# Performance work log

Measured on AMD Instinct MI355X. Metric: run time of the kernel, lower is better.

The kernel has to match this reference:

```python
import jax, jax.numpy as jnp
import numpy as np

N = 50000   # nodes
E = 500000  # edges
H = 128     # hidden_dim


def setup_inputs() -> dict:
    key = jax.random.key(0)
    ks = jax.random.split(key, 8)
    w = lambda k, shp: jax.random.normal(k, shp, jnp.float32) * 0.02
    return {
        "edge_idx": jax.random.randint(ks[0], (E, 2), 0, N, dtype=jnp.int32),
        "node_feats": jax.random.normal(ks[1], (N, H), jnp.float32),
        "edge_feats": jax.random.normal(ks[2], (E, H), jnp.float32),
        # edge MLP params: Linear(3H,H) -> ReLU -> Linear(H,H) -> LayerNorm(H)
        "We1": w(ks[3], (3 * H, H)), "be1": jnp.zeros((H,), jnp.float32),
        "We2": w(ks[4], (H, H)),     "be2": jnp.zeros((H,), jnp.float32),
        "ge": jnp.ones((H,), jnp.float32), "bge": jnp.zeros((H,), jnp.float32),
        # node MLP params: Linear(2H,H) -> ReLU -> Linear(H,H) -> LayerNorm(H)
        "Wn1": w(ks[5], (2 * H, H)), "bn1": jnp.zeros((H,), jnp.float32),
        "Wn2": w(ks[6], (H, H)),     "bn2": jnp.zeros((H,), jnp.float32),
        "gn": jnp.ones((H,), jnp.float32), "bgn": jnp.zeros((H,), jnp.float32),
    }


def layer_norm(x, g, b, eps=1e-5):
    m = jnp.mean(x, axis=-1, keepdims=True)
    v = jnp.var(x, axis=-1, keepdims=True)
    return (x - m) * jax.lax.rsqrt(v + eps) * g + b


def reference(edge_idx, node_feats, edge_feats,
              We1, be1, We2, be2, ge, bge,
              Wn1, bn1, Wn2, bn2, gn, bgn):
    senders = edge_idx[:, 0]
    receivers = edge_idx[:, 1]
    # edge update: gather endpoints, concat with edge feats, MLP + LN
    e_in = jnp.concatenate([node_feats[senders], node_feats[receivers], edge_feats], axis=-1)  # [E, 3H]
    edge_update = layer_norm(jax.nn.relu(e_in @ We1 + be1) @ We2 + be2, ge, bge)               # [E, H]
    # faithful to source: scatter-add of edge_feats (NOT edge_update) into receivers
    acc = jax.ops.segment_sum(edge_feats, receivers, num_segments=node_feats.shape[0])          # [N, H]
    n_in = jnp.concatenate([node_feats, acc], axis=-1)                                          # [N, 2H]
    node_update = layer_norm(jax.nn.relu(n_in @ Wn1 + bn1) @ Wn2 + bn2, gn, bgn)                # [N, H]
    return node_feats + node_update, edge_feats + edge_update
```

## Files before the change

kernel.cpp:

```cpp
#include <hip/hip_runtime.h>
#include <hip/hip_bf16.h>

#define DI __device__ __forceinline__

typedef __attribute__((ext_vector_type(8))) short short8;
typedef __attribute__((ext_vector_type(4))) short short4v;
typedef __attribute__((ext_vector_type(4))) float floatx4;

constexpr int NN = 50000;
constexpr int NE = 500000;
constexpr int H  = 128;
constexpr int NB1 = (NN + 255) / 256;

constexpr size_t OFF_BF   = 262144;
constexpr size_t OFF_PS   = 327680;
constexpr size_t OFF_PR   = 13127680;
constexpr size_t OFF_CNT  = 25927680;
constexpr size_t OFF_TMP  = 26127680;
constexpr size_t OFF_RS   = 26327680;
constexpr size_t OFF_CUR  = 26527680;
constexpr size_t OFF_BSUM = 26727680;
constexpr size_t OFF_CSR  = 26728704;

constexpr int WF_TOTAL = 131072;
constexpr int BIASF_FLOATS = 8*2048;

DI short f2bf(float f){ __bf16 b = (__bf16)f; return __builtin_bit_cast(short, b); }
DI float bf2f(short s){ return __builtin_bit_cast(float, ((unsigned)(unsigned short)s) << 16); }

__global__ __launch_bounds__(256) void zero_cnt_kernel(int* __restrict__ cnt){
  int i = blockIdx.x*256 + threadIdx.x;
  if (i < NN) cnt[i] = 0;
}

__global__ __launch_bounds__(256) void prep_kernel(
    const float* __restrict__ We1, const float* __restrict__ We2,
    const float* __restrict__ Wn1, const float* __restrict__ Wn2,
    const float* __restrict__ be1, const float* __restrict__ be2,
    const float* __restrict__ ge,  const float* __restrict__ bge,
    const float* __restrict__ bn1, const float* __restrict__ bn2,
    const float* __restrict__ gn,  const float* __restrict__ bgn,
    short* __restrict__ wf, float* __restrict__ bf)
{
  int t = blockIdx.x*256 + threadIdx.x;
  if (t < WF_TOTAL) {
    int blk = t >> 14, u = t & 16383;
    int j = u & 7, l = (u>>3)&63, nt = (u>>9)&7, ks = u>>12;
    const float* src; int roff; bool blayout = false;
    switch (blk) {
      case 0: src = We1; roff = 0;   break;
      case 1: src = We1; roff = 128; break;
      case 2: src = We1; roff = 256; break;
      case 3: src = We2; roff = 0;   break;
      case 4: src = Wn1; roff = 0;   break;
      case 5: src = Wn1; roff = 128; break;
      case 6: src = Wn2; roff = 0;   break;
      default: src = We2; roff = 0; blayout = true; break;
    }
    int row = blayout ? (32*ks + 16*(j>>2) + 4*(l>>4) + (j&3))
                      : (roff + 32*ks + 8*(l>>4) + j);
    int col = 16*nt + (l&15);
    wf[t] = f2bf(src[row*H + col]);
  } else if (t < WF_TOTAL + BIASF_FLOATS) {
    int tb = t - WF_TOTAL;
    int arr = tb >> 11, u = tb & 2047;
    int r = u&3, l = (u>>2)&63, mt = u>>8;
    int feat = 16*mt + 4*(l>>4) + r;
    const float* s;
    switch (arr) {
      case 0: s = be1; break; case 1: s = be2; break;
      case 2: s = ge;  break; case 3: s = bge; break;
      case 4: s = bn1; break; case 5: s = bn2; break;
      case 6: s = gn;  break; default: s = bgn; break;
    }
    bf[tb] = s[feat];
  }
}

__global__ __launch_bounds__(256) void hist_kernel(const int* __restrict__ ei, int* __restrict__ cnt){
  int e = blockIdx.x*256 + threadIdx.x;
  if (e < NE) atomicAdd(&cnt[ei[2*e+1]], 1);
}

__global__ __launch_bounds__(256) void scan1_kernel(const int* __restrict__ cnt,
                                                    int* __restrict__ tmp, int* __restrict__ blocksum){
  __shared__ int s[256];
  int t = threadIdx.x, i = blockIdx.x*256 + t;
  int v = (i < NN) ? cnt[i] : 0;
  s[t] = v; __syncthreads();
#pragma unroll
  for (int o=1; o<256; o<<=1){
    int u = (t >= o) ? s[t-o] : 0;
    __syncthreads();
    s[t] += u;
    __syncthreads();
  }
  if (i < NN) tmp[i] = s[t];
  if (t == 255) blocksum[blockIdx.x] = s[255];
}

__global__ __launch_bounds__(256) void scan2_kernel(int* __restrict__ blocksum){
  __shared__ int s[256];
  int t = threadIdx.x;
  int v = (t < NB1) ? blocksum[t] : 0;
  s[t] = v; __syncthreads();
#pragma unroll
  for (int o=1; o<256; o<<=1){
    int u = (t >= o) ? s[t-o] : 0;
    __syncthreads();
    s[t] += u;
    __syncthreads();
  }
  if (t < NB1) blocksum[t] = s[t] - v;
}

__global__ __launch_bounds__(256) void scan3_kernel(const int* __restrict__ cnt, const int* __restrict__ tmp,
                                                    const int* __restrict__ blocksum,
                                                    int* __restrict__ rowstart, int* __restrict__ cursor){
  int i = blockIdx.x*256 + threadIdx.x;
  if (i < NN){
    int rs = tmp[i] - cnt[i] + blocksum[blockIdx.x];
    rowstart[i] = rs; cursor[i] = rs;
  }
}

__global__ __launch_bounds__(256) void scatter_kernel(const int* __restrict__ ei,
                                                      int* __restrict__ cursor, int* __restrict__ csr){
  int e = blockIdx.x*256 + threadIdx.x;
  if (e < NE){
    int r = ei[2*e+1];
    int p = atomicAdd(&cursor[r], 1);
    csr[p] = e;
  }
}

__global__ __launch_bounds__(256) void segsum_kernel(const int* __restrict__ csr,
                                                     const int* __restrict__ rowstart,
                                                     const int* __restrict__ cnt,
                                                     const float* __restrict__ edge_feats,
                                                     float* __restrict__ acc){
  int tid = threadIdx.x;
  int w = tid>>6, l = tid&63;
  int hh = l>>5, q = l&31;
  int n = blockIdx.x*8 + w*2 + hh;
  if (n >= NN) return;
  int start = rowstart[n], deg = cnt[n];
  floatx4 s = floatx4{0.f,0.f,0.f,0.f};
  int k = 0;
  for (; k+4 <= deg; k += 4){
    int e0 = csr[start+k],   e1 = csr[start+k+1];
    int e2 = csr[start+k+2], e3 = csr[start+k+3];
    floatx4 v0 = *(const floatx4*)(edge_feats + (size_t)e0*H + 4*q);
    floatx4 v1 = *(const floatx4*)(edge_feats + (size_t)e1*H + 4*q);
    floatx4 v2 = *(const floatx4*)(edge_feats + (size_t)e2*H + 4*q);
    floatx4 v3 = *(const floatx4*)(edge_feats + (size_t)e3*H + 4*q);
    s += v0; s += v1; s += v2; s += v3;
  }
  for (; k < deg; ++k){
    int e = csr[start+k];
    s += *(const floatx4*)(edge_feats + (size_t)e*H + 4*q);
  }
  *(floatx4*)(acc + (size_t)n*H + 4*q) = s;
}

__global__ __launch_bounds__(256) void pproj_kernel(
    const float* __restrict__ node_feats,
    const short* __restrict__ wsf, const short* __restrict__ wrf,
    const float* __restrict__ b1f,
    short* __restrict__ Ps, short* __restrict__ Pr)
{
  const int tid = threadIdx.x;
  const int w = tid>>6, l = tid&63, g = l>>4, lo = l&15;
  int row = blockIdx.x*64 + w*16 + lo;
  bool valid = row < NN;
  int rowc = valid ? row : (NN-1);
  const float* sp = node_feats + (size_t)rowc*H;

  short8 ein[4];
#pragma unroll
  for (int ks=0; ks<4; ++ks){
    const int koff = ks*32 + g*8;
    floatx4 f0 = *(const floatx4*)(sp + koff);
    floatx4 f1 = *(const floatx4*)(sp + koff + 4);
    ein[ks][0]=f2bf(f0[0]); ein[ks][1]=f2bf(f0[1]); ein[ks][2]=f2bf(f0[2]); ein[ks][3]=f2bf(f0[3]);
    ein[ks][4]=f2bf(f1[0]); ein[ks][5]=f2bf(f1[1]); ein[ks][6]=f2bf(f1[2]); ein[ks][7]=f2bf(f1[3]);
  }

  floatx4 as[8], ar[8];
#pragma unroll
  for (int mt=0; mt<8; ++mt){ as[mt] = floatx4{0,0,0,0}; ar[mt] = floatx4{0,0,0,0}; }
#pragma unroll
  for (int ks=0; ks<4; ++ks){
#pragma unroll
    for (int mt=0; mt<8; ++mt){
      short8 wv = *(const short8*)(wsf + ((ks*8+mt)*64 + l)*8);
      as[mt] = __builtin_amdgcn_mfma_f32_16x16x32_bf16(wv, ein[ks], as[mt], 0,0,0);
      short8 wv2 = *(const short8*)(wrf + ((ks*8+mt)*64 + l)*8);
      ar[mt] = __builtin_amdgcn_mfma_f32_16x16x32_bf16(wv2, ein[ks], ar[mt], 0,0,0);
    }
  }

  if (valid){
    short* ps = Ps + (size_t)rowc*H + g*32;
    short* pr = Pr + (size_t)rowc*H + g*32;
#pragma unroll
    for (int mt=0; mt<8; ++mt){
      floatx4 bv = *(const floatx4*)(b1f + (mt*64+l)*4);
      short4v vs, vr;
#pragma unroll
      for (int r=0; r<4; ++r){ vs[r] = f2bf(as[mt][r] + bv[r]); vr[r] = f2bf(ar[mt][r]); }
      *(short4v*)(ps + mt*4) = vs;
      *(short4v*)(pr + mt*4) = vr;
    }
  }
}

template<int R>
__global__ __launch_bounds__(1024) void edge_kernel(
    const int* __restrict__ edge_idx,
    const float* __restrict__ edge_feats,
    const short* __restrict__ Ps, const short* __restrict__ Pr,
    const short* __restrict__ wef, const short* __restrict__ w2fB,
    const float* __restrict__ b2f,
    const float* __restrict__ gf,  const float* __restrict__ bgf,
    float* __restrict__ out_edge)
{
  extern __shared__ short smem[];
  short* wA = smem;
  short* wB = smem + 16384;
  const int tid = threadIdx.x;
  const int w = tid>>6, l = tid&63, g = l>>4, lo = l&15;

  int rowc[R]; bool valid[R]; int2 se[R];
#pragma unroll
  for (int b=0; b<R; ++b){
    int row = blockIdx.x*(16*16*R) + w*(16*R) + b*16 + lo;
    valid[b] = row < NE;
    rowc[b]  = valid[b] ? row : (NE-1);
    se[b] = *(const int2*)(edge_idx + 2*rowc[b]);
  }

  short8 vs[4], vr[4];
  {
    const short* ps = Ps + (size_t)se[0].x*H + g*32;
    const short* pr = Pr + (size_t)se[0].y*H + g*32;
#pragma unroll
    for (int m2=0; m2<4; ++m2){
      vs[m2] = *(const short8*)(ps + m2*8);
      vr[m2] = *(const short8*)(pr + m2*8);
    }
  }

#pragma unroll
  for (int rnd=0; rnd<2; ++rnd){
    int o = (rnd*1024 + tid)*8;
    *(short8*)(wA + o) = *(const short8*)(wef  + o);
    *(short8*)(wB + o) = *(const short8*)(w2fB + o);
  }
  __syncthreads();

#pragma unroll
  for (int b=0; b<R; ++b){
    floatx4 acc[8];
#pragma unroll
    for (int mt=0; mt<8; ++mt) acc[mt] = floatx4{0.f,0.f,0.f,0.f};

    const float* sp = edge_feats + (size_t)rowc[b]*H;
#pragma unroll
    for (int ks=0; ks<4; ++ks){
      const int koff = ks*32 + g*8;
      floatx4 f0 = *(const floatx4*)(sp + koff);
      floatx4 f1 = *(const floatx4*)(sp + koff + 4);
      short8 ein;
      ein[0]=f2bf(f0[0]); ein[1]=f2bf(f0[1]); ein[2]=f2bf(f0[2]); ein[3]=f2bf(f0[3]);
      ein[4]=f2bf(f1[0]); ein[5]=f2bf(f1[1]); ein[6]=f2bf(f1[2]); ein[7]=f2bf(f1[3]);
#pragma unroll
      for (int mt=0; mt<8; ++mt){
        short8 wv = *(const short8*)(wA + ((ks*8+mt)*64 + l)*8);
        acc[mt] = __builtin_amdgcn_mfma_f32_16x16x32_bf16(wv, ein, acc[mt], 0,0,0);
      }
    }

#pragma unroll
    for (int m2=0; m2<4; ++m2)
#pragma unroll
      for (int r=0; r<4; ++r){
        acc[2*m2][r]   += bf2f(vs[m2][r])   + bf2f(vr[m2][r]);
        acc[2*m2+1][r] += bf2f(vs[m2][4+r]) + bf2f(vr[m2][4+r]);
      }

    if (b+1 < R){
      const short* ps = Ps + (size_t)se[b+1].x*H + g*32;
      const short* pr = Pr + (size_t)se[b+1].y*H + g*32;
#pragma unroll
      for (int m2=0; m2<4; ++m2){
        vs[m2] = *(const short8*)(ps + m2*8);
        vr[m2] = *(const short8*)(pr + m2*8);
      }
    }

    short8 hb[4];
#pragma unroll
    for (int s=0; s<4; ++s){
#pragma unroll
      for (int r=0; r<4; ++r){
        float v0 = acc[2*s][r];
        float v1 = acc[2*s+1][r];
        hb[s][r]   = f2bf(v0 > 0.f ? v0 : 0.f);
        hb[s][4+r] = f2bf(v1 > 0.f ? v1 : 0.f);
      }
    }

#pragma unroll
    for (int mt=0; mt<8; ++mt) acc[mt] = *(const floatx4*)(b2f + (mt*64+l)*4);

#pragma unroll
    for (int s=0; s<4; ++s){
#pragma unroll
      for (int mt=0; mt<8; ++mt){
        short8 wv = *(const short8*)(wB + ((s*8+mt)*64 + l)*8);
        acc[mt] = __builtin_amdgcn_mfma_f32_16x16x32_bf16(wv, hb[s], acc[mt], 0,0,0);
      }
    }

    float sum = 0.f, ssq = 0.f;
#pragma unroll
    for (int mt=0; mt<8; ++mt)
#pragma unroll
      for (int r=0; r<4; ++r){ float v = acc[mt][r]; sum += v; ssq += v*v; }
    sum += __shfl_xor(sum, 16); ssq += __shfl_xor(ssq, 16);
    sum += __shfl_xor(sum, 32); ssq += __shfl_xor(ssq, 32);
    const float mean = sum * (1.f/H);
    const float var  = ssq * (1.f/H) - mean*mean;
    const float rs   = rsqrtf(var + 1e-5f);

    const float* resid = edge_feats + (size_t)rowc[b]*H;
    float* outp = out_edge + (size_t)rowc[b]*H;
#pragma unroll
    for (int mt=0; mt<8; ++mt){
      floatx4 gv  = *(const floatx4*)(gf  + (mt*64+l)*4);
      floatx4 bgv = *(const floatx4*)(bgf + (mt*64+l)*4);
      floatx4 ef  = *(const floatx4*)(resid + mt*16 + g*4);
      floatx4 o;
#pragma unroll
      for (int r=0; r<4; ++r) o[r] = ef[r] + (acc[mt][r]-mean)*rs*gv[r] + bgv[r];
      if (valid[b]) *(floatx4*)(outp + mt*16 + g*4) = o;
    }
  }
}

__global__ __launch_bounds__(256) void node_kernel(
    const float* __restrict__ node_feats,
    const short* __restrict__ w1f, const short* __restrict__ w2f,
    const float* __restrict__ b1f, const float* __restrict__ b2f,
    const float* __restrict__ gf,  const float* __restrict__ bgf,
    float* __restrict__ out_node)
{
  __shared__ short lds_h[4*2048];
  const int tid = threadIdx.x;
  const int w = tid>>6, l = tid&63, g = l>>4, lo = l&15;
  short* ldsw = lds_h + w*2048;

  int row = blockIdx.x*64 + w*16 + lo;
  bool valid = row < NN;
  int rowc = valid ? row : (NN-1);
  const float* sp0 = node_feats + (size_t)rowc*H;
  const float* sp1 = out_node   + (size_t)rowc*H;

  floatx4 acc1[8];
#pragma unroll
  for (int mt=0; mt<8; ++mt) acc1[mt] = *(const floatx4*)(b1f + (mt*64+l)*4);

#pragma unroll
  for (int ks=0; ks<8; ++ks){
    const float* sp = (ks<4) ? sp0 : sp1;
    const int koff = (ks&3)*32 + g*8;
    floatx4 f0 = *(const floatx4*)(sp + koff);
    floatx4 f1 = *(const floatx4*)(sp + koff + 4);
    short8 ein;
    ein[0]=f2bf(f0[0]); ein[1]=f2bf(f0[1]); ein[2]=f2bf(f0[2]); ein[3]=f2bf(f0[3]);
    ein[4]=f2bf(f1[0]); ein[5]=f2bf(f1[1]); ein[6]=f2bf(f1[2]); ein[7]=f2bf(f1[3]);
#pragma unroll
    for (int mt=0; mt<8; ++mt){
      short8 wv = *(const short8*)(w1f + ((ks*8+mt)*64 + l)*8);
      acc1[mt] = __builtin_amdgcn_mfma_f32_16x16x32_bf16(wv, ein, acc1[mt], 0,0,0);
    }
  }

#pragma unroll
  for (int mt=0; mt<8; ++mt){
    short4v hv;
#pragma unroll
    for (int r=0; r<4; ++r){
      float v = acc1[mt][r];
      hv[r] = f2bf(v > 0.f ? v : 0.f);
    }
    int off = (lo*256 + mt*32 + g*8) ^ ((lo&7)<<4);
    *(short4v*)((char*)ldsw + off) = hv;
  }

  floatx4 acc2[8];
#pragma unroll
  for (int mt=0; mt<8; ++mt) acc2[mt] = *(const floatx4*)(b2f + (mt*64+l)*4);

#pragma unroll
  for (int s=0; s<4; ++s){
    int roff = (lo*256 + s*64 + g*16) ^ ((lo&7)<<4);
    short8 hb = *(const short8*)((char*)ldsw + roff);
#pragma unroll
    for (int mt=0; mt<8; ++mt){
      short8 wv = *(const short8*)(w2f + ((s*8+mt)*64 + l)*8);
      acc2[mt] = __builtin_amdgcn_mfma_f32_16x16x32_bf16(wv, hb, acc2[mt], 0,0,0);
    }
  }

  float sum = 0.f, ssq = 0.f;
#pragma unroll
  for (int mt=0; mt<8; ++mt)
#pragma unroll
    for (int r=0; r<4; ++r){ float v = acc2[mt][r]; sum += v; ssq += v*v; }
  sum += __shfl_xor(sum, 16); ssq += __shfl_xor(ssq, 16);
  sum += __shfl_xor(sum, 32); ssq += __shfl_xor(ssq, 32);
  const float mean = sum * (1.f/H);
  const float var  = ssq * (1.f/H) - mean*mean;
  const float rs   = rsqrtf(var + 1e-5f);

#pragma unroll
  for (int mt=0; mt<8; ++mt){
    floatx4 gv  = *(const floatx4*)(gf  + (mt*64+l)*4);
    floatx4 bgv = *(const floatx4*)(bgf + (mt*64+l)*4);
    floatx4 nf  = *(const floatx4*)(node_feats + (size_t)rowc*H + mt*16 + g*4);
    floatx4 o;
#pragma unroll
    for (int r=0; r<4; ++r) o[r] = nf[r] + (acc2[mt][r]-mean)*rs*gv[r] + bgv[r];
    if (valid) *(floatx4*)(out_node + (size_t)rowc*H + mt*16 + g*4) = o;
  }
}

extern "C" void kernel_launch(void* const* d_in, const int* in_sizes, int n_in,
                              void* d_out, int out_size, void* d_ws, size_t ws_size,
                              hipStream_t stream)
{
  const int*   edge_idx   = (const int*)  d_in[0];
  const float* node_feats = (const float*)d_in[1];
  const float* edge_feats = (const float*)d_in[2];
  const float* We1=(const float*)d_in[3];  const float* be1=(const float*)d_in[4];
  const float* We2=(const float*)d_in[5];  const float* be2=(const float*)d_in[6];
  const float* ge =(const float*)d_in[7];  const float* bge=(const float*)d_in[8];
  const float* Wn1=(const float*)d_in[9];  const float* bn1=(const float*)d_in[10];
  const float* Wn2=(const float*)d_in[11]; const float* bn2=(const float*)d_in[12];
  const float* gn =(const float*)d_in[13]; const float* bgn=(const float*)d_in[14];

  float* out_node = (float*)d_out;
  float* out_edge = out_node + (size_t)NN*H;

  char* ws = (char*)d_ws;
  short* wf      = (short*)ws;
  float* bf      = (float*)(ws + OFF_BF);
  short* Ps      = (short*)(ws + OFF_PS);
  short* Pr      = (short*)(ws + OFF_PR);
  int* cnt       = (int*)(ws + OFF_CNT);
  int* tmp       = (int*)(ws + OFF_TMP);
  int* rowstart  = (int*)(ws + OFF_RS);
  int* cursor    = (int*)(ws + OFF_CUR);
  int* blocksum  = (int*)(ws + OFF_BSUM);
  int* csr       = (int*)(ws + OFF_CSR);

  short* wsf  = wf;
  short* wrf  = wf + 16384;
  short* wef  = wf + 32768;
  short* wn1f = wf + 65536;
  short* wn2f = wf + 98304;
  short* w2fB = wf + 114688;
  float* b1f  = bf;         float* b2f  = bf + 2048;
  float* gef  = bf + 4096;  float* bgef = bf + 6144;
  float* bn1f = bf + 8192;  float* bn2f = bf + 10240;
  float* gnf  = bf + 12288; float* bgnf = bf + 14336;

  zero_cnt_kernel<<<NB1, 256, 0, stream>>>(cnt);
  prep_kernel<<<(WF_TOTAL + BIASF_FLOATS + 255)/256, 256, 0, stream>>>(
      We1, We2, Wn1, Wn2, be1, be2, ge, bge, bn1, bn2, gn, bgn, wf, bf);

  hist_kernel<<<(NE+255)/256, 256, 0, stream>>>(edge_idx, cnt);
  scan1_kernel<<<NB1, 256, 0, stream>>>(cnt, tmp, blocksum);
  scan2_kernel<<<1, 256, 0, stream>>>(blocksum);
  scan3_kernel<<<NB1, 256, 0, stream>>>(cnt, tmp, blocksum, rowstart, cursor);
  scatter_kernel<<<(NE+255)/256, 256, 0, stream>>>(edge_idx, cursor, csr);

  pproj_kernel<<<(NN+63)/64, 256, 0, stream>>>(node_feats, wsf, wrf, b1f, Ps, Pr);

  edge_kernel<2><<<(NE + 511)/512, 1024, 65536, stream>>>(
      edge_idx, edge_feats, Ps, Pr, wef, w2fB, b2f, gef, bgef, out_edge);

  segsum_kernel<<<(NN+7)/8, 256, 0, stream>>>(csr, rowstart, cnt, edge_feats, out_node);

  node_kernel<<<(NN+63)/64, 256, 0, stream>>>(
      node_feats, wn1f, wn2f, bn1f, bn2f, gnf, bgnf, out_node);
}
```

Measured before the change: 382.2 us.

## Fuse segment-sum into edge kernel via interleaved block roles and prefetch edge feats

Merges the edge MLP kernel and the segment-sum kernel into one launch. Every fourth block runs the edge path and the other blocks run the segment sum over 32 nodes each. The edge path now processes 4 row groups per block instead of 2, and it prefetches the next group's edge features into registers while the current group's MFMAs run. The intent is to overlap gather-bound segment-sum traffic with MFMA-bound edge work and remove one launch. In exchange the code carries more register pressure, and segment-sum blocks request 64KB of dynamic LDS they never use, which may reduce occupancy.

```diff
diff --git a/kernel.cpp b/kernel.cpp
--- a/kernel.cpp
+++ b/kernel.cpp
@@ -24,6 +24,11 @@
 
 constexpr int WF_TOTAL = 131072;
 constexpr int BIASF_FLOATS = 8*2048;
+
+constexpr int R_EDGE   = 4;
+constexpr int EB_EDGE  = (NE + 1023) / 1024;
+constexpr int SEG_BLKS = (NN + 31) / 32;
+constexpr int FUSED_GRID = 2084;
 
 DI short f2bf(float f){ __bf16 b = (__bf16)f; return __builtin_bit_cast(short, b); }
 DI float bf2f(short s){ return __builtin_bit_cast(float, ((unsigned)(unsigned short)s) << 16); }
@@ -134,35 +139,6 @@
   }
 }
 
-__global__ __launch_bounds__(256) void segsum_kernel(const int* __restrict__ csr,
-                                                     const int* __restrict__ rowstart,
-                                                     const int* __restrict__ cnt,
-                                                     const float* __restrict__ edge_feats,
-                                                     float* __restrict__ acc){
-  int tid = threadIdx.x;
-  int w = tid>>6, l = tid&63;
-  int hh = l>>5, q = l&31;
-  int n = blockIdx.x*8 + w*2 + hh;
-  if (n >= NN) return;
-  int start = rowstart[n], deg = cnt[n];
-  floatx4 s = floatx4{0.f,0.f,0.f,0.f};
-  int k = 0;
-  for (; k+4 <= deg; k += 4){
-    int e0 = csr[start+k],   e1 = csr[start+k+1];
-    int e2 = csr[start+k+2], e3 = csr[start+k+3];
-    floatx4 v0 = *(const floatx4*)(edge_feats + (size_t)e0*H + 4*q);
-    floatx4 v1 = *(const floatx4*)(edge_feats + (size_t)e1*H + 4*q);
-    floatx4 v2 = *(const floatx4*)(edge_feats + (size_t)e2*H + 4*q);
-    floatx4 v3 = *(const floatx4*)(edge_feats + (size_t)e3*H + 4*q);
-    s += v0; s += v1; s += v2; s += v3;
-  }
-  for (; k < deg; ++k){
-    int e = csr[start+k];
-    s += *(const floatx4*)(edge_feats + (size_t)e*H + 4*q);
-  }
-  *(floatx4*)(acc + (size_t)n*H + 4*q) = s;
-}
-
 __global__ __launch_bounds__(256) void pproj_kernel(
     const float* __restrict__ node_feats,
     const short* __restrict__ wsf, const short* __restrict__ wrf,
@@ -215,29 +191,68 @@
   }
 }
 
-template<int R>
-__global__ __launch_bounds__(1024) void edge_kernel(
+__global__ __launch_bounds__(1024) void fused_kernel(
     const int* __restrict__ edge_idx,
     const float* __restrict__ edge_feats,
     const short* __restrict__ Ps, const short* __restrict__ Pr,
     const short* __restrict__ wef, const short* __restrict__ w2fB,
     const float* __restrict__ b2f,
     const float* __restrict__ gf,  const float* __restrict__ bgf,
-    float* __restrict__ out_edge)
+    float* __restrict__ out_edge,
+    const int* __restrict__ csr, const int* __restrict__ rowstart,
+    const int* __restrict__ cnt, float* __restrict__ acc_out)
 {
   extern __shared__ short smem[];
+  const int bid = blockIdx.x;
+  const int tid = threadIdx.x;
+
+  if ((bid & 3) != 0) {
+    int sb = bid - (bid>>2) - 1;
+    int w = tid>>6, l = tid&63;
+    int hh = l>>5, q = l&31;
+    int n = sb*32 + w*2 + hh;
+    if (n >= NN) return;
+    int start = rowstart[n], deg = cnt[n];
+    floatx4 s = floatx4{0.f,0.f,0.f,0.f};
+    int k = 0;
+    for (; k+4 <= deg; k += 4){
+      int e0 = csr[start+k],   e1 = csr[start+k+1];
+      int e2 = csr[start+k+2], e3 = csr[start+k+3];
+      floatx4 v0 = *(const floatx4*)(edge_feats + (size_t)e0*H + 4*q);
+      floatx4 v1 = *(const floatx4*)(edge_feats + (size_t)e1*H + 4*q);
+      floatx4 v2 = *(const floatx4*)(edge_feats + (size_t)e2*H + 4*q);
+      floatx4 v3 = *(const floatx4*)(edge_feats + (size_t)e3*H + 4*q);
+      s += v0; s += v1; s += v2; s += v3;
+    }
+    for (; k < deg; ++k){
+      int e = csr[start+k];
+      s += *(const floatx4*)(edge_feats + (size_t)e*H + 4*q);
+    }
+    *(floatx4*)(acc_out + (size_t)n*H + 4*q) = s;
+    return;
+  }
+
+  int eb = bid >> 2;
+  if (eb >= EB_EDGE) return;
+  constexpr int R = R_EDGE;
   short* wA = smem;
   short* wB = smem + 16384;
-  const int tid = threadIdx.x;
   const int w = tid>>6, l = tid&63, g = l>>4, lo = l&15;
 
   int rowc[R]; bool valid[R]; int2 se[R];
 #pragma unroll
   for (int b=0; b<R; ++b){
-    int row = blockIdx.x*(16*16*R) + w*(16*R) + b*16 + lo;
+    int row = eb*(16*16*R) + w*(16*R) + b*16 + lo;
     valid[b] = row < NE;
     rowc[b]  = valid[b] ? row : (NE-1);
     se[b] = *(const int2*)(edge_idx + 2*rowc[b]);
+  }
+
+#pragma unroll
+  for (int rnd=0; rnd<2; ++rnd){
+    int o = (rnd*1024 + tid)*8;
+    *(short8*)(wA + o) = *(const short8*)(wef  + o);
+    *(short8*)(wB + o) = *(const short8*)(w2fB + o);
   }
 
   short8 vs[4], vr[4];
@@ -250,34 +265,46 @@
       vr[m2] = *(const short8*)(pr + m2*8);
     }
   }
-
-#pragma unroll
-  for (int rnd=0; rnd<2; ++rnd){
-    int o = (rnd*1024 + tid)*8;
-    *(short8*)(wA + o) = *(const short8*)(wef  + o);
-    *(short8*)(wB + o) = *(const short8*)(w2fB + o);
+  floatx4 ef[8];
+  {
+    const float* sp = edge_feats + (size_t)rowc[0]*H;
+#pragma unroll
+    for (int ks=0; ks<4; ++ks){
+      ef[2*ks]   = *(const floatx4*)(sp + ks*32 + g*8);
+      ef[2*ks+1] = *(const floatx4*)(sp + ks*32 + g*8 + 4);
+    }
   }
   __syncthreads();
 
 #pragma unroll
   for (int b=0; b<R; ++b){
+    short8 ein[4];
+#pragma unroll
+    for (int ks=0; ks<4; ++ks){
+      ein[ks][0]=f2bf(ef[2*ks][0]);   ein[ks][1]=f2bf(ef[2*ks][1]);
+      ein[ks][2]=f2bf(ef[2*ks][2]);   ein[ks][3]=f2bf(ef[2*ks][3]);
+      ein[ks][4]=f2bf(ef[2*ks+1][0]); ein[ks][5]=f2bf(ef[2*ks+1][1]);
+      ein[ks][6]=f2bf(ef[2*ks+1][2]); ein[ks][7]=f2bf(ef[2*ks+1][3]);
+    }
+
+    if (b+1 < R){
+      const float* sp = edge_feats + (size_t)rowc[b+1]*H;
+#pragma unroll
+      for (int ks=0; ks<4; ++ks){
+        ef[2*ks]   = *(const floatx4*)(sp + ks*32 + g*8);
+        ef[2*ks+1] = *(const floatx4*)(sp + ks*32 + g*8 + 4);
+      }
+    }
+
     floatx4 acc[8];
 #pragma unroll
     for (int mt=0; mt<8; ++mt) acc[mt] = floatx4{0.f,0.f,0.f,0.f};
-
-    const float* sp = edge_feats + (size_t)rowc[b]*H;
 #pragma unroll
     for (int ks=0; ks<4; ++ks){
-      const int koff = ks*32 + g*8;
-      floatx4 f0 = *(const floatx4*)(sp + koff);
-      floatx4 f1 = *(const floatx4*)(sp + koff + 4);
-      short8 ein;
-      ein[0]=f2bf(f0[0]); ein[1]=f2bf(f0[1]); ein[2]=f2bf(f0[2]); ein[3]=f2bf(f0[3]);
-      ein[4]=f2bf(f1[0]); ein[5]=f2bf(f1[1]); ein[6]=f2bf(f1[2]); ein[7]=f2bf(f1[3]);
 #pragma unroll
       for (int mt=0; mt<8; ++mt){
         short8 wv = *(const short8*)(wA + ((ks*8+mt)*64 + l)*8);
-        acc[mt] = __builtin_amdgcn_mfma_f32_16x16x32_bf16(wv, ein, acc[mt], 0,0,0);
+        acc[mt] = __builtin_amdgcn_mfma_f32_16x16x32_bf16(wv, ein[ks], acc[mt], 0,0,0);
       }
     }
 
@@ -313,7 +340,6 @@
 
 #pragma unroll
     for (int mt=0; mt<8; ++mt) acc[mt] = *(const floatx4*)(b2f + (mt*64+l)*4);
-
 #pragma unroll
     for (int s=0; s<4; ++s){
 #pragma unroll
@@ -340,10 +366,10 @@
     for (int mt=0; mt<8; ++mt){
       floatx4 gv  = *(const floatx4*)(gf  + (mt*64+l)*4);
       floatx4 bgv = *(const floatx4*)(bgf + (mt*64+l)*4);
-      floatx4 ef  = *(const floatx4*)(resid + mt*16 + g*4);
+      floatx4 efr = *(const floatx4*)(resid + mt*16 + g*4);
       floatx4 o;
 #pragma unroll
-      for (int r=0; r<4; ++r) o[r] = ef[r] + (acc[mt][r]-mean)*rs*gv[r] + bgv[r];
+      for (int r=0; r<4; ++r) o[r] = efr[r] + (acc[mt][r]-mean)*rs*gv[r] + bgv[r];
       if (valid[b]) *(floatx4*)(outp + mt*16 + g*4) = o;
     }
   }
@@ -489,10 +515,9 @@
 
   pproj_kernel<<<(NN+63)/64, 256, 0, stream>>>(node_feats, wsf, wrf, b1f, Ps, Pr);
 
-  edge_kernel<2><<<(NE + 511)/512, 1024, 65536, stream>>>(
-      edge_idx, edge_feats, Ps, Pr, wef, w2fB, b2f, gef, bgef, out_edge);
-
-  segsum_kernel<<<(NN+7)/8, 256, 0, stream>>>(csr, rowstart, cnt, edge_feats, out_node);
+  fused_kernel<<<FUSED_GRID, 1024, 65536, stream>>>(
+      edge_idx, edge_feats, Ps, Pr, wef, w2fB, b2f, gef, bgef, out_edge,
+      csr, rowstart, cnt, out_node);
 
   node_kernel<<<(NN+63)/64, 256, 0, stream>>>(
       node_feats, wn1f, wn2f, bn1f, bn2f, gnf, bgnf, out_node);
```

After: 904.2 us. +136.6%, slower.
